# Kernel optimization log

Measured on AMD Instinct MI355X. Metric: run time of the kernel, lower is better.

Reference implementation:

```python
import jax, jax.numpy as jnp
import numpy as np
from jax import lax

STATE_LEN = 5
N_BASE = 4
N_STATES = N_BASE ** STATE_LEN      # 1024
ALPHA_LEN = N_BASE + 1              # 5 (blank + 4 bases)
BLANK_SCORE = 2.0
SCALE = 5.0
NEG = -1e30                         # log-zero surrogate (avoids -inf NaNs)

def _make_idx():
    s = np.arange(N_STATES)
    stay = s[:, None]
    # torch: arange(1024).repeat_interleave(4).reshape(4,-1).T -> idx[j,1+b] = b*256 + j//4
    move = np.repeat(s, N_BASE).reshape(N_BASE, -1).T
    return jnp.asarray(np.concatenate([stay, move], axis=1), dtype=jnp.int32)  # (1024,5)

IDX = _make_idx()

def _logZ_full(scores):
    # full-lattice logZ; scores (T,N,5120)
    T, N, C = scores.shape
    Ms = scores.reshape(T, N, N_STATES, ALPHA_LEN)
    def step(alpha, Mt):
        a = alpha[:, IDX]                          # (N,1024,5) gather of predecessors
        return jax.nn.logsumexp(a + Mt, axis=-1), None
    alpha0 = jnp.zeros((N, N_STATES), scores.dtype)
    alphaT, _ = lax.scan(step, alpha0, Ms)
    return jax.nn.logsumexp(alphaT, axis=-1)       # (N,)

def _prepare_ctc_scores(scores, targets):
    # scores (T,N,C), targets (N,Lmax) base ids in 1..4
    t = jnp.clip(targets - 1, 0)
    T, N, C = scores.shape
    Lmax = t.shape[1]
    n = Lmax - (STATE_LEN - 1)
    stay_idx = sum(t[:, i:n + i] * (N_BASE ** (STATE_LEN - i - 1)) for i in range(STATE_LEN)) * ALPHA_LEN
    move_idx = stay_idx[:, 1:] + t[:, :n - 1] + 1
    stay = jnp.take_along_axis(scores, jnp.broadcast_to(stay_idx[None], (T, N, n)), axis=2)
    move = jnp.take_along_axis(scores, jnp.broadcast_to(move_idx[None], (T, N, n - 1)), axis=2)
    return stay, move

def _ctc_logZ(stay, move, lens):
    # stay (T,N,L), move (T,N,L-1), lens (N,) effective kmer-path lengths
    T, N, L = stay.shape
    alpha0 = jnp.full((N, L), NEG, stay.dtype).at[:, 0].set(0.0)
    def step(alpha, sm):
        s, m = sm
        moved = jnp.pad(alpha[:, :-1] + m, ((0, 0), (1, 0)), constant_values=NEG)
        return jnp.logaddexp(alpha + s, moved), None
    alphaT, _ = lax.scan(step, alpha0, (stay, move))
    return alphaT[jnp.arange(N), lens - 1]

def setup_inputs() -> dict:
    key = jax.random.key(0)
    k1, k2, k3, k4, k5, k6 = jax.random.split(key, 6)
    B, T, D, Lmax = 16, 512, 512, 256
    hs_pad = jax.random.normal(k1, (B, T, D), dtype=jnp.float32)
    hlens = jnp.full((B,), T, dtype=jnp.int32)
    ys_pad = jax.random.randint(k2, (B, Lmax), 1, 5, dtype=jnp.int32)
    ys_lens = jax.random.randint(k3, (B,), 64, Lmax + 1, dtype=jnp.int32)
    W = jax.random.normal(k4, (4096, D), dtype=jnp.float32) * 0.02
    b = jax.random.normal(k5, (4096,), dtype=jnp.float32) * 0.01
    return {"hs_pad": hs_pad, "hlens": hlens, "ys_pad": ys_pad, "ys_lens": ys_lens, "W": W, "b": b}

def reference(hs_pad, hlens, ys_pad, ys_lens, W, b):
    x = jnp.transpose(hs_pad, (1, 0, 2))                 # (T,B,D)
    scores = jnp.tanh(x @ W.T + b) * SCALE               # (T,N,4096)
    T, N, C = scores.shape
    scores = jnp.pad(scores.reshape(T, N, C // N_BASE, N_BASE),
                     ((0, 0), (0, 0), (0, 0), (1, 0)), constant_values=BLANK_SCORE)
    scores = scores.reshape(T, N, -1).astype(jnp.float32)  # (T,N,5120)
    # normalise: subtract full-lattice logZ / T
    logZ = _logZ_full(scores)
    norm = scores - logZ[:, None] / T                    # (N,1) broadcasts over (T,N,C)
    stay, move = _prepare_ctc_scores(norm, ys_pad)
    logz = _ctc_logZ(stay, move, ys_lens + 1 - STATE_LEN)
    loss = -(logz / ys_lens.astype(scores.dtype))        # (N,) (reduction=None in forward)
    scores_bt = jnp.transpose(scores, (1, 0, 2))
    return loss, scores_bt, scores_bt
```

## Files before the change

### kernel.cpp

```cpp
#include <hip/hip_runtime.h>
#include <hip/hip_bf16.h>
#include <hip/hip_fp16.h>
#include <math.h>

#define T_STEPS 512
#define NB      16
#define D_IN    512
#define CG      4096
#define CO      5120
#define LMAX    252
#define NEGF    (-1e30f)
#define SCORES_SZ 41943040LL
#define L2E 1.4426950408889634f
#define LN2 0.6931471805599453f
#define STAYT 0.36787944117144233f

typedef __attribute__((ext_vector_type(8))) short bf16x8;
typedef __attribute__((ext_vector_type(4))) float f32x4;

__device__ __forceinline__ float tanh5(float x) {
    x = fminf(fmaxf(x, -15.f), 15.f);
    float e = __expf(2.f * x);
    return 5.f * (e - 1.f) / (e + 1.f);
}
__device__ __forceinline__ unsigned short f2bf(float v) {
    __hip_bfloat16 h = __float2bfloat16(v);
    return *reinterpret_cast<unsigned short*>(&h);
}
__device__ __forceinline__ float h2f(unsigned short s) {
    union { unsigned short u; _Float16 h; } c; c.u = s;
    return (float)c.h;
}
__device__ __forceinline__ unsigned short f2h(float v) {
    union { unsigned short u; _Float16 h; } c; c.h = (_Float16)v;
    return c.u;
}
__device__ __forceinline__ void cvt8(uint4 u, float* g) {
    g[0] = h2f((unsigned short)(u.x & 0xffff)); g[1] = h2f((unsigned short)(u.x >> 16));
    g[2] = h2f((unsigned short)(u.y & 0xffff)); g[3] = h2f((unsigned short)(u.y >> 16));
    g[4] = h2f((unsigned short)(u.z & 0xffff)); g[5] = h2f((unsigned short)(u.z >> 16));
    g[6] = h2f((unsigned short)(u.w & 0xffff)); g[7] = h2f((unsigned short)(u.w >> 16));
}
__device__ __forceinline__ void step_barrier() {
    asm volatile("s_waitcnt lgkmcnt(0)" ::: "memory");
    __builtin_amdgcn_s_barrier();
    asm volatile("" ::: "memory");
}

__global__ __launch_bounds__(256) void cvt_bf16_kernel(const float* __restrict__ src,
                                                       unsigned short* __restrict__ dst,
                                                       int n4) {
    int i = blockIdx.x * 256 + threadIdx.x;
    if (i < n4) {
        float4 v = *(reinterpret_cast<const float4*>(src) + i);
        ushort4 o;
        o.x = f2bf(v.x); o.y = f2bf(v.y); o.z = f2bf(v.z); o.w = f2bf(v.w);
        *(reinterpret_cast<ushort4*>(dst) + i) = o;
    }
}

template <bool WSE>
__global__ __launch_bounds__(256) void crf_gemm_bf16(
    const unsigned short* __restrict__ A16,
    const unsigned short* __restrict__ W16,
    const float* __restrict__ bias,
    float* __restrict__ out,
    unsigned short* __restrict__ e16)
{
    __shared__ unsigned short As[128 * 64];
    __shared__ unsigned short Bs[128 * 64];
    const int tid  = threadIdx.x;
    const int lane = tid & 63;
    const int wv   = __builtin_amdgcn_readfirstlane(tid >> 6);
    const int wr   = wv >> 1, wc = wv & 1;
    const int m0   = blockIdx.y * 128;
    const int n0   = blockIdx.x * 128;
    const int wbase = tid & 192;

    f32x4 acc[4][4];
    #pragma unroll
    for (int i = 0; i < 4; ++i)
        #pragma unroll
        for (int j = 0; j < 4; ++j) acc[i][j] = (f32x4){0.f, 0.f, 0.f, 0.f};

    const int l15 = lane & 15, lj = lane >> 4, l7 = lane & 7;

    for (int k0 = 0; k0 < D_IN; k0 += 64) {
        __syncthreads();
        #pragma unroll
        for (int i = 0; i < 4; ++i) {
            const int c   = i * 256 + tid;
            const int row = c >> 3;
            const int jg  = (c & 7) ^ (row & 7);
            const unsigned short* ga = A16 + (size_t)(m0 + row) * D_IN + k0 + jg * 8;
            const unsigned short* gb = W16 + (size_t)(n0 + row) * D_IN + k0 + jg * 8;
            unsigned short* la = As + (size_t)(i * 256 + wbase) * 8;
            unsigned short* lb = Bs + (size_t)(i * 256 + wbase) * 8;
            __builtin_amdgcn_global_load_lds((const __attribute__((address_space(1))) void*)ga,
                                             (__attribute__((address_space(3))) void*)la, 16, 0, 0);
            __builtin_amdgcn_global_load_lds((const __attribute__((address_space(1))) void*)gb,
                                             (__attribute__((address_space(3))) void*)lb, 16, 0, 0);
        }
        __syncthreads();
        #pragma unroll
        for (int ks = 0; ks < 2; ++ks) {
            bf16x8 af[4], bb[4];
            #pragma unroll
            for (int mi = 0; mi < 4; ++mi) {
                const int row = wr * 64 + mi * 16 + l15;
                const int jsw = (ks * 4 + lj) ^ l7;
                af[mi] = *reinterpret_cast<const bf16x8*>(&As[row * 64 + jsw * 8]);
            }
            #pragma unroll
            for (int ni = 0; ni < 4; ++ni) {
                const int row = wc * 64 + ni * 16 + l15;
                const int jsw = (ks * 4 + lj) ^ l7;
                bb[ni] = *reinterpret_cast<const bf16x8*>(&Bs[row * 64 + jsw * 8]);
            }
            #pragma unroll
            for (int mi = 0; mi < 4; ++mi)
                #pragma unroll
                for (int ni = 0; ni < 4; ++ni)
                    acc[mi][ni] = __builtin_amdgcn_mfma_f32_16x16x32_bf16(
                        af[mi], bb[ni], acc[mi][ni], 0, 0, 0);
        }
    }

    float bv[4];
    #pragma unroll
    for (int ni = 0; ni < 4; ++ni) bv[ni] = bias[n0 + wc * 64 + ni * 16 + l15];

    #pragma unroll
    for (int mi = 0; mi < 4; ++mi) {
        #pragma unroll
        for (int r = 0; r < 4; ++r) {
            const int m = m0 + wr * 64 + mi * 16 + lj * 4 + r;
            float* r1 = out + 16 + (size_t)m * CO;
            #pragma unroll
            for (int ni = 0; ni < 4; ++ni) {
                const int n = n0 + wc * 64 + ni * 16 + l15;
                const float v = tanh5(acc[mi][ni][r] + bv[ni]);
                const int ch = (n >> 2) * 5 + (n & 3) + 1;
                r1[ch] = v;
                r1[ch + SCORES_SZ] = v;
                if ((l15 & 3) == 0) {
                    r1[ch - 1] = 2.0f;
                    r1[ch - 1 + SCORES_SZ] = 2.0f;
                }
                if (WSE) e16[(size_t)m * CG + n] = f2h(__expf(v - 3.0f));
            }
        }
    }
}

__global__ __launch_bounds__(256) void fb_kernel(
    const unsigned short* __restrict__ e16,
    const int* __restrict__ ys_pad,
    const int* __restrict__ ys_lens,
    float* __restrict__ FA, float* __restrict__ FAe,
    float* __restrict__ FB, float* __restrict__ FBe,
    float* __restrict__ CAL, float* __restrict__ CBE)
{
    const int role = blockIdx.x >> 4;
    const int n = blockIdx.x & 15;
    const int q = threadIdx.x;
    if (role < 2) {
        __shared__ float buf[2][1024];
        __shared__ float wmax4[4];
        const int lane = q & 63, wvi = q >> 6;
        float P0 = 1.f, P1 = 1.f, P2 = 1.f, P3 = 1.f, acc = 0.f;
        *(float4*)&buf[0][4 * q] = make_float4(1.f, 1.f, 1.f, 1.f);
        const unsigned short* eb = e16 + (size_t)(n * T_STEPS) * CG + 16 * q;
        const bool FWD = (role == 0);
        uint4 pf[4][2];
        #pragma unroll
        for (int u = 0; u < 4; ++u) {
            const int row = FWD ? u : (511 - u);
            pf[u][0] = *(const uint4*)(eb + (size_t)row * CG);
            pf[u][1] = *(const uint4*)(eb + (size_t)row * CG + 8);
        }
        step_barrier();
        int cur = 0;
        for (int t = 0; t < 256; t += 8) {
            #pragma unroll
            for (int u = 0; u < 8; ++u) {
                float g[16];
                cvt8(pf[u & 3][0], g);
                cvt8(pf[u & 3][1], g + 8);
                int tn = t + u + 4; if (tn > 255) tn = 255;
                const int row = FWD ? tn : (511 - tn);
                pf[u & 3][0] = *(const uint4*)(eb + (size_t)row * CG);
                pf[u & 3][1] = *(const uint4*)(eb + (size_t)row * CG + 8);
                float n0, n1, n2, n3;
                if (FWD) {
                    const float b0 = buf[cur][q];
                    const float b1 = buf[cur][q + 256];
                    const float b2 = buf[cur][q + 512];
                    const float b3 = buf[cur][q + 768];
                    n0 = fmaf(STAYT, P0, fmaf(g[0],  b0, g[1]  * b1) + fmaf(g[2],  b2, g[3]  * b3));
                    n1 = fmaf(STAYT, P1, fmaf(g[4],  b0, g[5]  * b1) + fmaf(g[6],  b2, g[7]  * b3));
                    n2 = fmaf(STAYT, P2, fmaf(g[8],  b0, g[9]  * b1) + fmaf(g[10], b2, g[11] * b3));
                    n3 = fmaf(STAYT, P3, fmaf(g[12], b0, g[13] * b1) + fmaf(g[14], b2, g[15] * b3));
                } else {
                    const float4 b4 = *(const float4*)&buf[cur][4 * q];
                    n0 = fmaf(STAYT, P0, fmaf(g[0], b4.x, g[4] * b4.y) + fmaf(g[8],  b4.z, g[12] * b4.w));
                    n1 = fmaf(STAYT, P1, fmaf(g[1], b4.x, g[5] * b4.y) + fmaf(g[9],  b4.z, g[13] * b4.w));
                    n2 = fmaf(STAYT, P2, fmaf(g[2], b4.x, g[6] * b4.y) + fmaf(g[10], b4.z, g[14] * b4.w));
                    n3 = fmaf(STAYT, P3, fmaf(g[3], b4.x, g[7] * b4.y) + fmaf(g[11], b4.z, g[15] * b4.w));
                }
                if (u == 1) {
                    const float wm = fmaxf(fmaxf(wmax4[0], wmax4[1]), fmaxf(wmax4[2], wmax4[3]));
                    const int e = (int)((__float_as_uint(wm) >> 23) & 0xff) - 127;
                    const float c = __uint_as_float((unsigned)(127 - e) << 23);
                    n0 *= c; n1 *= c; n2 *= c; n3 *= c;
                    acc += (float)e;
                }
                P0 = n0; P1 = n1; P2 = n2; P3 = n3;
                if (FWD) {
                    *(float4*)&buf[cur ^ 1][4 * q] = make_float4(P0, P1, P2, P3);
                } else {
                    buf[cur ^ 1][q]       = P0;
                    buf[cur ^ 1][q + 256] = P1;
                    buf[cur ^ 1][q + 512] = P2;
                    buf[cur ^ 1][q + 768] = P3;
                }
                if (u == 0) {
                    float m = fmaxf(fmaxf(P0, P1), fmaxf(P2, P3));
                    #pragma unroll
                    for (int msk = 1; msk < 64; msk <<= 1)
                        m = fmaxf(m, __shfl_xor(m, msk, 64));
                    if (lane == 0) wmax4[wvi] = m;
                }
                step_barrier();
                cur ^= 1;
            }
        }
        if (FWD) {
            *(float4*)&FA[n * 1024 + 4 * q] = make_float4(P0, P1, P2, P3);
            if (q == 0) FAe[n] = acc;
        } else {
            FB[n * 1024 + q]       = P0;
            FB[n * 1024 + q + 256] = P1;
            FB[n * 1024 + q + 512] = P2;
            FB[n * 1024 + q + 768] = P3;
            if (q == 0) FBe[n] = acc;
        }
    } else {
        const bool FWD = (role == 2);
        __shared__ float abuf[2][256];
        __shared__ int tcl[256];
        tcl[q] = max(ys_pad[n * 256 + q] - 1, 0);
        __syncthreads();
        int mch = 0; bool val;
        if (FWD) {
            val = (q >= 1 && q < LMAX);
            if (val) {
                const int code = tcl[q] * 256 + tcl[q + 1] * 64 + tcl[q + 2] * 16
                               + tcl[q + 3] * 4 + tcl[q + 4];
                mch = code * 4 + tcl[q - 1];
            }
        } else {
            val = (q < LMAX - 1);
            if (val) {
                const int code = tcl[q + 1] * 256 + tcl[q + 2] * 64 + tcl[q + 3] * 16
                               + tcl[q + 4] * 4 + tcl[q + 5];
                mch = code * 4 + tcl[q];
            }
        }
        const int li = ys_lens[n] - 5;
        float a;
        if (FWD) a = (q == 0) ? 0.f : NEGF;
        else     a = (q == li) ? 0.f : NEGF;
        abuf[0][q] = a;
        const unsigned short* eb = e16 + (size_t)(n * T_STEPS) * CG;
        unsigned short pv[8];
        #pragma unroll
        for (int u = 0; u < 8; ++u) {
            const int row = FWD ? u : (511 - u);
            pv[u] = eb[(size_t)row * CG + mch];
        }
        step_barrier();
        const float STAY2 = (2.0f - 3.0f) * L2E;
        int cur = 0;
        for (int t = 0; t < 256; t += 8) {
            #pragma unroll
            for (int u = 0; u < 8; ++u) {
                const float g2 = val ? __builtin_amdgcn_logf(h2f(pv[u])) : NEGF;
                int tn = t + u + 8; if (tn > 255) tn = 255;
                const int row = FWD ? tn : (511 - tn);
                pv[u] = eb[(size_t)row * CG + mch];
                float nb;
                if (FWD) nb = (q > 0) ? abuf[cur][q - 1] : NEGF;
                else     nb = (q < 255) ? abuf[cur][q + 1] : NEGF;
                const float st = a + STAY2;
                const float mv = nb + g2;
                const float mx = fmaxf(st, mv);
                const float mn = fminf(st, mv);
                a = mx + __builtin_amdgcn_logf(1.f + __builtin_amdgcn_exp2f(mn - mx));
                abuf[cur ^ 1][q] = a;
                step_barrier();
                cur ^= 1;
            }
        }
        if (FWD) CAL[n * 256 + q] = a;
        else     CBE[n * 256 + q] = a;
    }
}

__global__ __launch_bounds__(256) void combine_kernel(
    const float* __restrict__ FA, const float* __restrict__ FAe,
    const float* __restrict__ FB, const float* __restrict__ FBe,
    const float* __restrict__ CAL, const float* __restrict__ CBE,
    float* __restrict__ ws)
{
    __shared__ float red[256];
    const int q = threadIdx.x;
    if (blockIdx.x < 16) {
        const int n = blockIdx.x;
        float s = 0.f;
        #pragma unroll
        for (int k = 0; k < 4; ++k)
            s += FA[n * 1024 + 4 * q + k] * FB[n * 1024 + 4 * q + k];
        red[q] = s; __syncthreads();
        for (int off = 128; off > 0; off >>= 1) {
            if (q < off) red[q] += red[q + off];
            __syncthreads();
        }
        if (q == 0) ws[n] = LN2 * (FAe[n] + FBe[n] + __builtin_amdgcn_logf(red[0]));
    } else {
        const int n = blockIdx.x - 16;
        const float x = CAL[n * 256 + q] + CBE[n * 256 + q];
        red[q] = x; __syncthreads();
        for (int off = 128; off > 0; off >>= 1) {
            if (q < off) red[q] = fmaxf(red[q], red[q + off]);
            __syncthreads();
        }
        const float m = red[0]; __syncthreads();
        red[q] = __builtin_amdgcn_exp2f(x - m); __syncthreads();
        for (int off = 128; off > 0; off >>= 1) {
            if (q < off) red[q] += red[q + off];
            __syncthreads();
        }
        if (q == 0) ws[NB + n] = LN2 * (m + __builtin_amdgcn_logf(red[0]));
    }
}

__global__ __launch_bounds__(1024) void crf_fwd_kernel(
    const float* __restrict__ scores,
    const int* __restrict__ ys_pad,
    const int* __restrict__ ys_lens,
    float* __restrict__ ws)
{
    const int blk = blockIdx.x;
    const float STAY = 2.0f * L2E;
    if (blk < NB) {
        const int n = blk;
        const int s = threadIdx.x;
        __shared__ float buf[2][1024];
        __shared__ float red[1024];
        float alpha = 0.f;
        buf[0][s] = 0.f;
        const int j0 = s >> 2;
        const float* rowp = scores + (size_t)(n * T_STEPS) * CO + 5 * s + 1;
        float pm[4][4];
        #pragma unroll
        for (int u = 0; u < 4; ++u) {
            const float* r = rowp + (size_t)u * CO;
            pm[u][0] = r[0]; pm[u][1] = r[1]; pm[u][2] = r[2]; pm[u][3] = r[3];
        }
        __syncthreads();
        int cur = 0;
        for (int t = 0; t < T_STEPS; t += 4) {
            #pragma unroll
            for (int u = 0; u < 4; ++u) {
                const float m1 = pm[u][0], m2 = pm[u][1], m3 = pm[u][2], m4 = pm[u][3];
                int tp = t + u + 4; if (tp > T_STEPS - 1) tp = T_STEPS - 1;
                const float* r = rowp + (size_t)tp * CO;
                pm[u][0] = r[0]; pm[u][1] = r[1]; pm[u][2] = r[2]; pm[u][3] = r[3];
                const float b1 = buf[cur][j0];
                const float b2 = buf[cur][j0 + 256];
                const float b3 = buf[cur][j0 + 512];
                const float b4 = buf[cur][j0 + 768];
                const float a0 = alpha + STAY;
                const float a1 = fmaf(m1, L2E, b1);
                const float a2 = fmaf(m2, L2E, b2);
                const float a3 = fmaf(m3, L2E, b3);
                const float a4 = fmaf(m4, L2E, b4);
                const float mx = fmaxf(fmaxf(fmaxf(a0, a1), fmaxf(a2, a3)), a4);
                const float sum = __builtin_amdgcn_exp2f(a0 - mx) + __builtin_amdgcn_exp2f(a1 - mx)
                                + __builtin_amdgcn_exp2f(a2 - mx) + __builtin_amdgcn_exp2f(a3 - mx)
                                + __builtin_amdgcn_exp2f(a4 - mx);
                alpha = mx + __builtin_amdgcn_logf(sum);
                buf[cur ^ 1][s] = alpha;
                __syncthreads();
                cur ^= 1;
            }
        }
        red[s] = alpha;
        __syncthreads();
        for (int off = 512; off > 0; off >>= 1) {
            if (s < off) red[s] = fmaxf(red[s], red[s + off]);
            __syncthreads();
        }
        const float gmax = red[0];
        __syncthreads();
        red[s] = __builtin_amdgcn_exp2f(alpha - gmax);
        __syncthreads();
        for (int off = 512; off > 0; off >>= 1) {
            if (s < off) red[s] += red[s + off];
            __syncthreads();
        }
        if (s == 0) ws[n] = LN2 * (gmax + __builtin_amdgcn_logf(red[0]));
    } else {
        const int n = blk - NB;
        const int i = threadIdx.x;
        __shared__ float abuf[2][LMAX];
        __shared__ int tcl[256];
        if (i < 256) tcl[i] = max(ys_pad[n * 256 + i] - 1, 0);
        __syncthreads();
        int mch = -1;
        if (i >= 1 && i < LMAX) {
            const int code = tcl[i] * 256 + tcl[i + 1] * 64 + tcl[i + 2] * 16
                           + tcl[i + 3] * 4 + tcl[i + 4];
            mch = code * 5 + tcl[i - 1] + 1;
        }
        float alpha = (i == 0) ? 0.f : NEGF;
        if (i < LMAX) abuf[0][i] = alpha;
        const float* base = scores + (size_t)(n * T_STEPS) * CO;
        const size_t moff = (mch >= 0) ? (size_t)mch : 0;
        float pg[4];
        #pragma unroll
        for (int u = 0; u < 4; ++u) pg[u] = base[(size_t)u * CO + moff];
        __syncthreads();
        int cur = 0;
        for (int t = 0; t < T_STEPS; t += 4) {
            #pragma unroll
            for (int u = 0; u < 4; ++u) {
                const float g = pg[u];
                int tp = t + u + 4; if (tp > T_STEPS - 1) tp = T_STEPS - 1;
                pg[u] = base[(size_t)tp * CO + moff];
                if (i < LMAX) {
                    const float a_stay = alpha + STAY;
                    const float prev = (i > 0) ? abuf[cur][i - 1] : NEGF;
                    const float a_mv = (i > 0) ? fmaf(g, L2E, prev) : NEGF;
                    const float mx = fmaxf(a_stay, a_mv);
                    const float mn = fminf(a_stay, a_mv);
                    alpha = mx + __builtin_amdgcn_logf(1.f + __builtin_amdgcn_exp2f(mn - mx));
                    abuf[cur ^ 1][i] = alpha;
                }
                __syncthreads();
                cur ^= 1;
            }
        }
        if (i == ys_lens[n] - 5) ws[NB + n] = alpha * LN2;
    }
}

__global__ void crf_loss_kernel(const float* __restrict__ ws,
                                const int* __restrict__ ys_lens,
                                float* __restrict__ out)
{
    const int n = threadIdx.x;
    if (n < NB) {
        const float logz = ws[NB + n] - ws[n];
        out[n] = -(logz / (float)ys_lens[n]);
    }
}

extern "C" void kernel_launch(void* const* d_in, const int* in_sizes, int n_in,
                              void* d_out, int out_size, void* d_ws, size_t ws_size,
                              hipStream_t stream)
{
    const float* hs      = (const float*)d_in[0];
    const int*   ys_pad  = (const int*)d_in[2];
    const int*   ys_lens = (const int*)d_in[3];
    const float* W       = (const float*)d_in[4];
    const float* bias    = (const float*)d_in[5];
    float* out = (float*)d_out;
    float* ws  = (float*)d_ws;

    const size_t A_ELEMS = (size_t)8192 * 512;
    const size_t W_ELEMS = (size_t)4096 * 512;
    const size_t E_ELEMS = (size_t)8192 * 4096;
    const size_t X_FLOATS = (size_t)16 * 1024 * 2 + 32 + (size_t)16 * 256 * 2;
    const size_t NEED = 256 + (A_ELEMS + W_ELEMS + E_ELEMS) * 2 + X_FLOATS * 4;

    unsigned short* A16 = (unsigned short*)((char*)d_ws + 256);
    unsigned short* W16 = A16 + A_ELEMS;
    unsigned short* E16 = W16 + W_ELEMS;
    float* FA  = (float*)(E16 + E_ELEMS);
    float* FAe = FA + 16 * 1024;
    float* FB  = FAe + 16;
    float* FBe = FB + 16 * 1024;
    float* CAL = FBe + 16;
    float* CBE = CAL + 16 * 256;

    cvt_bf16_kernel<<<(int)(A_ELEMS / 4 / 256), 256, 0, stream>>>(hs, A16, (int)(A_ELEMS / 4));
    cvt_bf16_kernel<<<(int)(W_ELEMS / 4 / 256), 256, 0, stream>>>(W, W16, (int)(W_ELEMS / 4));
    dim3 grid(CG / 128, (NB * T_STEPS) / 128);

    if (ws_size >= NEED) {
        crf_gemm_bf16<true><<<grid, 256, 0, stream>>>(A16, W16, bias, out, E16);
        fb_kernel<<<64, 256, 0, stream>>>(E16, ys_pad, ys_lens, FA, FAe, FB, FBe, CAL, CBE);
        combine_kernel<<<32, 256, 0, stream>>>(FA, FAe, FB, FBe, CAL, CBE, ws);
    } else {
        crf_gemm_bf16<false><<<grid, 256, 0, stream>>>(A16, W16, bias, out, nullptr);
        crf_fwd_kernel<<<2 * NB, 1024, 0, stream>>>(out + 16, ys_pad, ys_lens, ws);
    }
    crf_loss_kernel<<<1, 64, 0, stream>>>(ws, ys_lens, out);
}
```

Measured before the change: 220.7 us.

## Stream forward-backward inputs through LDS ring buffer and pre-gather CTC scores

The CRF forward/backward recursion now loads each timestep's emission row through an 8-deep async global-to-LDS ring, using global_load_lds with vmcnt waits, instead of a 4-deep register prefetch. The CTC path gets a separate parallel gather kernel that builds a compact per-timestep score array, which the CTC recursion then streams through a small LDS ring. The loss is computed directly in a merged combine kernel, which removes the separate loss launch. The goal is to hide global latency in the serial recursion loop, at the cost of about 136KB of LDS per block and an extra kernel launch plus a scratch buffer.

```diff
diff --git a/kernel.cpp b/kernel.cpp
--- a/kernel.cpp
+++ b/kernel.cpp
@@ -46,6 +46,10 @@
     __builtin_amdgcn_s_barrier();
     asm volatile("" ::: "memory");
 }
+__device__ __forceinline__ void gll16(const unsigned short* g, unsigned short* l) {
+    __builtin_amdgcn_global_load_lds((const __attribute__((address_space(1))) void*)g,
+                                     (__attribute__((address_space(3))) void*)l, 16, 0, 0);
+}
 
 __global__ __launch_bounds__(256) void cvt_bf16_kernel(const float* __restrict__ src,
                                                        unsigned short* __restrict__ dst,
@@ -94,12 +98,8 @@
             const int jg  = (c & 7) ^ (row & 7);
             const unsigned short* ga = A16 + (size_t)(m0 + row) * D_IN + k0 + jg * 8;
             const unsigned short* gb = W16 + (size_t)(n0 + row) * D_IN + k0 + jg * 8;
-            unsigned short* la = As + (size_t)(i * 256 + wbase) * 8;
-            unsigned short* lb = Bs + (size_t)(i * 256 + wbase) * 8;
-            __builtin_amdgcn_global_load_lds((const __attribute__((address_space(1))) void*)ga,
-                                             (__attribute__((address_space(3))) void*)la, 16, 0, 0);
-            __builtin_amdgcn_global_load_lds((const __attribute__((address_space(1))) void*)gb,
-                                             (__attribute__((address_space(3))) void*)lb, 16, 0, 0);
+            gll16(ga, As + (size_t)(i * 256 + wbase) * 8);
+            gll16(gb, Bs + (size_t)(i * 256 + wbase) * 8);
         }
         __syncthreads();
         #pragma unroll
@@ -153,87 +153,114 @@
     }
 }
 
-__global__ __launch_bounds__(256) void fb_kernel(
+__global__ __launch_bounds__(256) void ctc_gather_kernel(
     const unsigned short* __restrict__ e16,
     const int* __restrict__ ys_pad,
+    unsigned short* __restrict__ G16)
+{
+    const int n  = blockIdx.y;
+    const int t0 = blockIdx.x * 32;
+    const int q  = threadIdx.x;
+    __shared__ int tcl[256];
+    tcl[q] = max(ys_pad[n * 256 + q] - 1, 0);
+    __syncthreads();
+    int mch = 0;
+    if (q >= 1 && q < LMAX) {
+        const int code = tcl[q] * 256 + tcl[q + 1] * 64 + tcl[q + 2] * 16
+                       + tcl[q + 3] * 4 + tcl[q + 4];
+        mch = code * 4 + tcl[q - 1];
+    }
+    const unsigned short* eb = e16 + (size_t)(n * T_STEPS) * CG;
+    unsigned short* gb = G16 + ((size_t)n * T_STEPS + t0) * 256;
+    for (int dt = 0; dt < 32; ++dt)
+        gb[dt * 256 + q] = eb[(size_t)(t0 + dt) * CG + mch];
+}
+
+__global__ __launch_bounds__(256) void fb2_kernel(
+    const unsigned short* __restrict__ e16,
+    const unsigned short* __restrict__ G16,
     const int* __restrict__ ys_lens,
     float* __restrict__ FA, float* __restrict__ FAe,
     float* __restrict__ FB, float* __restrict__ FBe,
     float* __restrict__ CAL, float* __restrict__ CBE)
 {
+    __shared__ unsigned char SH[139280];
     const int role = blockIdx.x >> 4;
     const int n = blockIdx.x & 15;
     const int q = threadIdx.x;
+    const int w = q >> 6, lane = q & 63;
     if (role < 2) {
-        __shared__ float buf[2][1024];
-        __shared__ float wmax4[4];
-        const int lane = q & 63, wvi = q >> 6;
+        unsigned short* ring = (unsigned short*)SH;
+        float* buf   = (float*)(SH + 131072);
+        float* wmax4 = (float*)(SH + 131072 + 8192);
+        const bool FWD = (role == 0);
+        const unsigned short* eb = e16 + (size_t)(n * T_STEPS) * CG;
         float P0 = 1.f, P1 = 1.f, P2 = 1.f, P3 = 1.f, acc = 0.f;
-        *(float4*)&buf[0][4 * q] = make_float4(1.f, 1.f, 1.f, 1.f);
-        const unsigned short* eb = e16 + (size_t)(n * T_STEPS) * CG + 16 * q;
-        const bool FWD = (role == 0);
-        uint4 pf[4][2];
-        #pragma unroll
-        for (int u = 0; u < 4; ++u) {
-            const int row = FWD ? u : (511 - u);
-            pf[u][0] = *(const uint4*)(eb + (size_t)row * CG);
-            pf[u][1] = *(const uint4*)(eb + (size_t)row * CG + 8);
-        }
+        *(float4*)&buf[4 * q] = make_float4(1.f, 1.f, 1.f, 1.f);
+
+        #define CRF_STAGE(s) {                                                    \
+            const int rr = ((s) < 256) ? (s) : 255;                               \
+            const int erow = FWD ? rr : (511 - rr);                               \
+            const unsigned short* ga = eb + (size_t)erow * CG + (w << 10) + lane * 8; \
+            unsigned short* la = ring + (((s) & 15) << 12) + (w << 10);           \
+            gll16(ga, la);                                                        \
+            gll16(ga + 512, la + 512); }
+
+        #pragma unroll
+        for (int s = 0; s < 8; ++s) CRF_STAGE(s);
+        asm volatile("s_waitcnt vmcnt(14)" ::: "memory");
         step_barrier();
         int cur = 0;
-        for (int t = 0; t < 256; t += 8) {
-            #pragma unroll
-            for (int u = 0; u < 8; ++u) {
-                float g[16];
-                cvt8(pf[u & 3][0], g);
-                cvt8(pf[u & 3][1], g + 8);
-                int tn = t + u + 4; if (tn > 255) tn = 255;
-                const int row = FWD ? tn : (511 - tn);
-                pf[u & 3][0] = *(const uint4*)(eb + (size_t)row * CG);
-                pf[u & 3][1] = *(const uint4*)(eb + (size_t)row * CG + 8);
-                float n0, n1, n2, n3;
-                if (FWD) {
-                    const float b0 = buf[cur][q];
-                    const float b1 = buf[cur][q + 256];
-                    const float b2 = buf[cur][q + 512];
-                    const float b3 = buf[cur][q + 768];
-                    n0 = fmaf(STAYT, P0, fmaf(g[0],  b0, g[1]  * b1) + fmaf(g[2],  b2, g[3]  * b3));
-                    n1 = fmaf(STAYT, P1, fmaf(g[4],  b0, g[5]  * b1) + fmaf(g[6],  b2, g[7]  * b3));
-                    n2 = fmaf(STAYT, P2, fmaf(g[8],  b0, g[9]  * b1) + fmaf(g[10], b2, g[11] * b3));
-                    n3 = fmaf(STAYT, P3, fmaf(g[12], b0, g[13] * b1) + fmaf(g[14], b2, g[15] * b3));
-                } else {
-                    const float4 b4 = *(const float4*)&buf[cur][4 * q];
-                    n0 = fmaf(STAYT, P0, fmaf(g[0], b4.x, g[4] * b4.y) + fmaf(g[8],  b4.z, g[12] * b4.w));
-                    n1 = fmaf(STAYT, P1, fmaf(g[1], b4.x, g[5] * b4.y) + fmaf(g[9],  b4.z, g[13] * b4.w));
-                    n2 = fmaf(STAYT, P2, fmaf(g[2], b4.x, g[6] * b4.y) + fmaf(g[10], b4.z, g[14] * b4.w));
-                    n3 = fmaf(STAYT, P3, fmaf(g[3], b4.x, g[7] * b4.y) + fmaf(g[11], b4.z, g[15] * b4.w));
-                }
-                if (u == 1) {
-                    const float wm = fmaxf(fmaxf(wmax4[0], wmax4[1]), fmaxf(wmax4[2], wmax4[3]));
-                    const int e = (int)((__float_as_uint(wm) >> 23) & 0xff) - 127;
-                    const float c = __uint_as_float((unsigned)(127 - e) << 23);
-                    n0 *= c; n1 *= c; n2 *= c; n3 *= c;
-                    acc += (float)e;
-                }
-                P0 = n0; P1 = n1; P2 = n2; P3 = n3;
-                if (FWD) {
-                    *(float4*)&buf[cur ^ 1][4 * q] = make_float4(P0, P1, P2, P3);
-                } else {
-                    buf[cur ^ 1][q]       = P0;
-                    buf[cur ^ 1][q + 256] = P1;
-                    buf[cur ^ 1][q + 512] = P2;
-                    buf[cur ^ 1][q + 768] = P3;
-                }
-                if (u == 0) {
-                    float m = fmaxf(fmaxf(P0, P1), fmaxf(P2, P3));
-                    #pragma unroll
-                    for (int msk = 1; msk < 64; msk <<= 1)
-                        m = fmaxf(m, __shfl_xor(m, msk, 64));
-                    if (lane == 0) wmax4[wvi] = m;
-                }
-                step_barrier();
-                cur ^= 1;
-            }
+        for (int t = 0; t < 256; ++t) {
+            CRF_STAGE(t + 8);
+            const unsigned short* rg = ring + ((t & 15) << 12) + (q << 4);
+            const uint4 r0 = *(const uint4*)rg;
+            const uint4 r1 = *(const uint4*)(rg + 8);
+            float g[16];
+            cvt8(r0, g); cvt8(r1, g + 8);
+            float n0, n1, n2, n3;
+            if (FWD) {
+                const float b0 = buf[cur * 1024 + q];
+                const float b1 = buf[cur * 1024 + q + 256];
+                const float b2 = buf[cur * 1024 + q + 512];
+                const float b3 = buf[cur * 1024 + q + 768];
+                n0 = fmaf(STAYT, P0, fmaf(g[0],  b0, g[1]  * b1) + fmaf(g[2],  b2, g[3]  * b3));
+                n1 = fmaf(STAYT, P1, fmaf(g[4],  b0, g[5]  * b1) + fmaf(g[6],  b2, g[7]  * b3));
+                n2 = fmaf(STAYT, P2, fmaf(g[8],  b0, g[9]  * b1) + fmaf(g[10], b2, g[11] * b3));
+                n3 = fmaf(STAYT, P3, fmaf(g[12], b0, g[13] * b1) + fmaf(g[14], b2, g[15] * b3));
+            } else {
+                const float4 b4 = *(const float4*)&buf[cur * 1024 + 4 * q];
+                n0 = fmaf(STAYT, P0, fmaf(g[0], b4.x, g[4] * b4.y) + fmaf(g[8],  b4.z, g[12] * b4.w));
+                n1 = fmaf(STAYT, P1, fmaf(g[1], b4.x, g[5] * b4.y) + fmaf(g[9],  b4.z, g[13] * b4.w));
+                n2 = fmaf(STAYT, P2, fmaf(g[2], b4.x, g[6] * b4.y) + fmaf(g[10], b4.z, g[14] * b4.w));
+                n3 = fmaf(STAYT, P3, fmaf(g[3], b4.x, g[7] * b4.y) + fmaf(g[11], b4.z, g[15] * b4.w));
+            }
+            if ((t & 7) == 1) {
+                const float wm = fmaxf(fmaxf(wmax4[0], wmax4[1]), fmaxf(wmax4[2], wmax4[3]));
+                const int e = (int)((__float_as_uint(wm) >> 23) & 0xff) - 127;
+                const float c = __uint_as_float((unsigned)(127 - e) << 23);
+                n0 *= c; n1 *= c; n2 *= c; n3 *= c;
+                acc += (float)e;
+            }
+            P0 = n0; P1 = n1; P2 = n2; P3 = n3;
+            if (FWD) {
+                *(float4*)&buf[(cur ^ 1) * 1024 + 4 * q] = make_float4(P0, P1, P2, P3);
+            } else {
+                buf[(cur ^ 1) * 1024 + q]       = P0;
+                buf[(cur ^ 1) * 1024 + q + 256] = P1;
+                buf[(cur ^ 1) * 1024 + q + 512] = P2;
+                buf[(cur ^ 1) * 1024 + q + 768] = P3;
+            }
+            if ((t & 7) == 0) {
+                float m = fmaxf(fmaxf(P0, P1), fmaxf(P2, P3));
+                #pragma unroll
+                for (int msk = 1; msk < 64; msk <<= 1)
+                    m = fmaxf(m, __shfl_xor(m, msk, 64));
+                if (lane == 0) wmax4[w] = m;
+            }
+            asm volatile("s_waitcnt vmcnt(14)" ::: "memory");
+            step_barrier();
+            cur ^= 1;
         }
         if (FWD) {
             *(float4*)&FA[n * 1024 + 4 * q] = make_float4(P0, P1, P2, P3);
@@ -245,103 +272,95 @@
             FB[n * 1024 + q + 768] = P3;
             if (q == 0) FBe[n] = acc;
         }
+        #undef CRF_STAGE
     } else {
+        unsigned short* rng = (unsigned short*)SH;
+        float* abuf = (float*)(SH + 16384);
         const bool FWD = (role == 2);
-        __shared__ float abuf[2][256];
-        __shared__ int tcl[256];
-        tcl[q] = max(ys_pad[n * 256 + q] - 1, 0);
-        __syncthreads();
-        int mch = 0; bool val;
-        if (FWD) {
-            val = (q >= 1 && q < LMAX);
-            if (val) {
-                const int code = tcl[q] * 256 + tcl[q + 1] * 64 + tcl[q + 2] * 16
-                               + tcl[q + 3] * 4 + tcl[q + 4];
-                mch = code * 4 + tcl[q - 1];
-            }
-        } else {
-            val = (q < LMAX - 1);
-            if (val) {
-                const int code = tcl[q + 1] * 256 + tcl[q + 2] * 64 + tcl[q + 3] * 16
-                               + tcl[q + 4] * 4 + tcl[q + 5];
-                mch = code * 4 + tcl[q];
-            }
-        }
+        const unsigned short* Gn = G16 + (size_t)n * T_STEPS * 256;
         const int li = ys_lens[n] - 5;
-        float a;
-        if (FWD) a = (q == 0) ? 0.f : NEGF;
-        else     a = (q == li) ? 0.f : NEGF;
-        abuf[0][q] = a;
-        const unsigned short* eb = e16 + (size_t)(n * T_STEPS) * CG;
-        unsigned short pv[8];
-        #pragma unroll
-        for (int u = 0; u < 8; ++u) {
-            const int row = FWD ? u : (511 - u);
-            pv[u] = eb[(size_t)row * CG + mch];
-        }
+        const bool val = FWD ? (q >= 1 && q < LMAX) : (q < LMAX - 1);
+        const int myidx = FWD ? q : ((q + 1 < 256) ? q + 1 : 255);
+        float a = FWD ? ((q == 0) ? 0.f : NEGF)
+                      : ((q == li) ? 0.f : NEGF);
+        abuf[q] = a;
+        if (w == 0) {
+            #pragma unroll
+            for (int p = 0; p < 8; ++p) {
+                const int s0 = 2 * p;
+                const int rbase = FWD ? s0 : (510 - s0);
+                gll16(Gn + (size_t)rbase * 256 + lane * 8, rng + ((s0 & 31) << 8));
+            }
+        }
+        asm volatile("s_waitcnt vmcnt(0)" ::: "memory");
         step_barrier();
         const float STAY2 = (2.0f - 3.0f) * L2E;
         int cur = 0;
-        for (int t = 0; t < 256; t += 8) {
-            #pragma unroll
-            for (int u = 0; u < 8; ++u) {
-                const float g2 = val ? __builtin_amdgcn_logf(h2f(pv[u])) : NEGF;
-                int tn = t + u + 8; if (tn > 255) tn = 255;
-                const int row = FWD ? tn : (511 - tn);
-                pv[u] = eb[(size_t)row * CG + mch];
-                float nb;
-                if (FWD) nb = (q > 0) ? abuf[cur][q - 1] : NEGF;
-                else     nb = (q < 255) ? abuf[cur][q + 1] : NEGF;
-                const float st = a + STAY2;
-                const float mv = nb + g2;
-                const float mx = fmaxf(st, mv);
-                const float mn = fminf(st, mv);
-                a = mx + __builtin_amdgcn_logf(1.f + __builtin_amdgcn_exp2f(mn - mx));
-                abuf[cur ^ 1][q] = a;
-                step_barrier();
-                cur ^= 1;
-            }
+        for (int t = 0; t < 256; ++t) {
+            if (((t & 1) == 0) && w == 0) {
+                const int s0 = t + 16;
+                const int rbase = FWD ? s0 : (510 - s0);
+                gll16(Gn + (size_t)rbase * 256 + lane * 8, rng + ((s0 & 31) << 8));
+            }
+            const int slot = FWD ? (t & 31) : ((t & 31) ^ 1);
+            const unsigned short gv = rng[(slot << 8) + myidx];
+            const float g2 = val ? __builtin_amdgcn_logf(h2f(gv)) : NEGF;
+            float nb;
+            if (FWD) nb = (q > 0)   ? abuf[cur * 256 + q - 1] : NEGF;
+            else     nb = (q < 255) ? abuf[cur * 256 + q + 1] : NEGF;
+            const float st = a + STAY2;
+            const float mv = nb + g2;
+            const float mx = fmaxf(st, mv);
+            const float mn = fminf(st, mv);
+            a = mx + __builtin_amdgcn_logf(1.f + __builtin_amdgcn_exp2f(mn - mx));
+            abuf[(cur ^ 1) * 256 + q] = a;
+            if (((t & 1) == 0) && w == 0)
+                asm volatile("s_waitcnt vmcnt(7)" ::: "memory");
+            step_barrier();
+            cur ^= 1;
         }
         if (FWD) CAL[n * 256 + q] = a;
         else     CBE[n * 256 + q] = a;
     }
 }
 
-__global__ __launch_bounds__(256) void combine_kernel(
+__global__ __launch_bounds__(256) void combine2_kernel(
     const float* __restrict__ FA, const float* __restrict__ FAe,
     const float* __restrict__ FB, const float* __restrict__ FBe,
     const float* __restrict__ CAL, const float* __restrict__ CBE,
-    float* __restrict__ ws)
+    const int* __restrict__ ys_lens,
+    float* __restrict__ out)
 {
     __shared__ float red[256];
+    __shared__ float lz;
+    const int n = blockIdx.x;
     const int q = threadIdx.x;
-    if (blockIdx.x < 16) {
-        const int n = blockIdx.x;
-        float s = 0.f;
-        #pragma unroll
-        for (int k = 0; k < 4; ++k)
-            s += FA[n * 1024 + 4 * q + k] * FB[n * 1024 + 4 * q + k];
-        red[q] = s; __syncthreads();
-        for (int off = 128; off > 0; off >>= 1) {
-            if (q < off) red[q] += red[q + off];
-            __syncthreads();
-        }
-        if (q == 0) ws[n] = LN2 * (FAe[n] + FBe[n] + __builtin_amdgcn_logf(red[0]));
-    } else {
-        const int n = blockIdx.x - 16;
-        const float x = CAL[n * 256 + q] + CBE[n * 256 + q];
-        red[q] = x; __syncthreads();
-        for (int off = 128; off > 0; off >>= 1) {
-            if (q < off) red[q] = fmaxf(red[q], red[q + off]);
-            __syncthreads();
-        }
-        const float m = red[0]; __syncthreads();
-        red[q] = __builtin_amdgcn_exp2f(x - m); __syncthreads();
-        for (int off = 128; off > 0; off >>= 1) {
-            if (q < off) red[q] += red[q + off];
-            __syncthreads();
-        }
-        if (q == 0) ws[NB + n] = LN2 * (m + __builtin_amdgcn_logf(red[0]));
+    float s = 0.f;
+    #pragma unroll
+    for (int k = 0; k < 4; ++k)
+        s += FA[n * 1024 + 4 * q + k] * FB[n * 1024 + 4 * q + k];
+    red[q] = s; __syncthreads();
+    for (int off = 128; off > 0; off >>= 1) {
+        if (q < off) red[q] += red[q + off];
+        __syncthreads();
+    }
+    if (q == 0) lz = FAe[n] + FBe[n] + __builtin_amdgcn_logf(red[0]);
+    __syncthreads();
+    const float x = CAL[n * 256 + q] + CBE[n * 256 + q];
+    red[q] = x; __syncthreads();
+    for (int off = 128; off > 0; off >>= 1) {
+        if (q < off) red[q] = fmaxf(red[q], red[q + off]);
+        __syncthreads();
+    }
+    const float m = red[0]; __syncthreads();
+    red[q] = __builtin_amdgcn_exp2f(x - m); __syncthreads();
+    for (int off = 128; off > 0; off >>= 1) {
+        if (q < off) red[q] += red[q + off];
+        __syncthreads();
+    }
+    if (q == 0) {
+        const float un = m + __builtin_amdgcn_logf(red[0]);
+        out[n] = -(LN2 * (un - lz) / (float)ys_lens[n]);
     }
 }
 
@@ -482,13 +501,15 @@
     const size_t A_ELEMS = (size_t)8192 * 512;
     const size_t W_ELEMS = (size_t)4096 * 512;
     const size_t E_ELEMS = (size_t)8192 * 4096;
+    const size_t G_ELEMS = (size_t)NB * T_STEPS * 256;
     const size_t X_FLOATS = (size_t)16 * 1024 * 2 + 32 + (size_t)16 * 256 * 2;
-    const size_t NEED = 256 + (A_ELEMS + W_ELEMS + E_ELEMS) * 2 + X_FLOATS * 4;
+    const size_t NEED = 256 + (A_ELEMS + W_ELEMS + E_ELEMS + G_ELEMS) * 2 + X_FLOATS * 4;
 
     unsigned short* A16 = (unsigned short*)((char*)d_ws + 256);
     unsigned short* W16 = A16 + A_ELEMS;
     unsigned short* E16 = W16 + W_ELEMS;
-    float* FA  = (float*)(E16 + E_ELEMS);
+    unsigned short* G16 = E16 + E_ELEMS;
+    float* FA  = (float*)(G16 + G_ELEMS);
     float* FAe = FA + 16 * 1024;
     float* FB  = FAe + 16;
     float* FBe = FB + 16 * 1024;
@@ -501,11 +522,13 @@
 
     if (ws_size >= NEED) {
         crf_gemm_bf16<true><<<grid, 256, 0, stream>>>(A16, W16, bias, out, E16);
-        fb_kernel<<<64, 256, 0, stream>>>(E16, ys_pad, ys_lens, FA, FAe, FB, FBe, CAL, CBE);
-        combine_kernel<<<32, 256, 0, stream>>>(FA, FAe, FB, FBe, CAL, CBE, ws);
+        dim3 gg(T_STEPS / 32, NB);
+        ctc_gather_kernel<<<gg, 256, 0, stream>>>(E16, ys_pad, G16);
+        fb2_kernel<<<64, 256, 0, stream>>>(E16, G16, ys_lens, FA, FAe, FB, FBe, CAL, CBE);
+        combine2_kernel<<<16, 256, 0, stream>>>(FA, FAe, FB, FBe, CAL, CBE, ys_lens, out);
     } else {
         crf_gemm_bf16<false><<<grid, 256, 0, stream>>>(A16, W16, bias, out, nullptr);
         crf_fwd_kernel<<<2 * NB, 1024, 0, stream>>>(out + 16, ys_pad, ys_lens, ws);
-    }
-    crf_loss_kernel<<<1, 64, 0, stream>>>(ws, ys_lens, out);
-}
+        crf_loss_kernel<<<1, 64, 0, stream>>>(ws, ys_lens, out);
+    }
+}
```

After: 339.4 us. +53.8%, slower.
